# Performance work log

Measured on AMD Instinct MI355X. Metric: run time of the kernel, lower is better.

Reference implementation:

```python
import jax, jax.numpy as jnp
import numpy as np

EPS = 1e-8  # torch.cosine_similarity default eps


def _gru_stack(x_seq, h0, w_ih, w_hh, b_ih, b_hh):
    """Multi-layer GRU with input_size=hidden_size=1, vectorized over N lanes.
    x_seq: [T, N], h0: [L, N], w_ih/w_hh/b_ih/b_hh: [L, 3] (gate order r, z, n).
    Returns (last-layer output seq [T, N], final hidden per layer [L, N])."""
    def layer_body(x_seq, p):
        wi, wh, bi, bh, h0_l = p
        def step(h, x):
            r = jax.nn.sigmoid(wi[0] * x + bi[0] + wh[0] * h + bh[0])
            z = jax.nn.sigmoid(wi[1] * x + bi[1] + wh[1] * h + bh[1])
            n = jnp.tanh(wi[2] * x + bi[2] + r * (wh[2] * h + bh[2]))
            h_new = (1.0 - z) * n + z * h
            return h_new, h_new
        h_fin, out = jax.lax.scan(step, h0_l, x_seq)
        return out, h_fin
    out_seq, h_fin = jax.lax.scan(layer_body, x_seq, (w_ih, w_hh, b_ih, b_hh, h0))
    return out_seq, h_fin


def _forward(inputs, w_ih, w_hh, b_ih, b_hh, horizon):
    B, _, nodes, T = inputs.shape
    L = w_ih.shape[0]  # == T (num_layers = seq_len)
    # [B,1,nodes,T] -> [T, nodes, B] -> [T, nodes*B]; GRU weights are shared
    # across nodes, so all per-node GRU calls batch into one.
    x = inputs[:, 0].transpose(2, 1, 0).reshape(T, nodes * B)
    h0 = jnp.zeros((L, nodes * B), inputs.dtype)
    out, h = _gru_stack(x, h0, w_ih, w_hh, b_ih, b_hh)
    # horizon-1 additional passes, feeding output back as input with carried h
    def hstep(carry, _):
        o, hh = carry
        o, hh = _gru_stack(o, hh, w_ih, w_hh, b_ih, b_hh)
        return (o, hh), None
    (out, h), _ = jax.lax.scan(hstep, (out, h), None, length=horizon - 1)
    hv = h.reshape(L, nodes, B)  # final hidden scalar per (layer, node, batch)
    # cosine similarity across the batch dim between every pair of nodes
    norms = jnp.maximum(jnp.linalg.norm(hv, axis=-1), EPS)  # [L, nodes]
    dots = jnp.einsum('lib,ljb->lij', hv, hv)               # [L, nodes, nodes]
    adj = dots / (norms[:, :, None] * norms[:, None, :])
    # h0_gru list-of-per-node tensors [L, B, 1] -> stacked [nodes, L, B, 1]
    h_out = hv.transpose(1, 0, 2)[..., None]
    return adj, h_out


def setup_inputs() -> dict:
    key = jax.random.key(0)
    ks = jax.random.split(key, 5)
    B, nodes, T, horizon = 16, 1024, 24, 8
    inputs = jax.random.normal(ks[0], (B, 1, nodes, T), dtype=jnp.float32)
    # PyTorch GRU init: U(-1/sqrt(hidden), 1/sqrt(hidden)) = U(-1, 1) here
    u = lambda k: jax.random.uniform(k, (T, 3), dtype=jnp.float32, minval=-1.0, maxval=1.0)
    return {"inputs": inputs, "w_ih": u(ks[1]), "w_hh": u(ks[2]),
            "b_ih": u(ks[3]), "b_hh": u(ks[4]), "horizon": horizon}


def reference(inputs, w_ih, w_hh, b_ih, b_hh, horizon):
    return _forward(inputs, w_ih, w_hh, b_ih, b_hh, horizon)
```

## Files before the change

kernel.cpp:

```cpp
#include <hip/hip_runtime.h>
#include <math.h>

#define NODES 1024
#define BATCH 16
#define TLEN 24
#define LAYERS 24
#define NLANES (NODES * BATCH)
#define LOG2E 1.44269504088896340736f

typedef float v2f __attribute__((ext_vector_type(2)));

#if __has_builtin(__builtin_amdgcn_rcpf)
__device__ __forceinline__ float fast_rcp(float x) { return __builtin_amdgcn_rcpf(x); }
#else
__device__ __forceinline__ float fast_rcp(float x) { return 1.0f / x; }
#endif

#if __has_builtin(__builtin_amdgcn_exp2f)
__device__ __forceinline__ float fast_exp2(float x) { return __builtin_amdgcn_exp2f(x); }
#else
__device__ __forceinline__ float fast_exp2(float x) { return exp2f(x); }
#endif

#if __has_builtin(__builtin_elementwise_fma)
__device__ __forceinline__ v2f pk_fma(v2f a, v2f b, v2f c) {
    return __builtin_elementwise_fma(a, b, c);
}
#else
__device__ __forceinline__ v2f pk_fma(v2f a, v2f b, v2f c) {
    v2f d; d.x = fmaf(a.x, b.x, c.x); d.y = fmaf(a.y, b.y, c.y); return d;
}
#endif

struct GruK2 { v2f rW, rU, rC, zW, zU, zC, nW, nC, nU, nD; };
struct GruKs { float rW, rU, rC, zW, zU, zC, nW, nC, nU, nD; };

__device__ __forceinline__ GruK2 make_k2(
    const float* __restrict__ w_ih, const float* __restrict__ w_hh,
    const float* __restrict__ b_ih, const float* __restrict__ b_hh,
    int la, int lb)
{
    GruK2 K;
    #pragma unroll
    for (int s = 0; s < 2; ++s) {
        const int l = s ? lb : la;
        K.rW[s] = -LOG2E * w_ih[l*3+0]; K.rU[s] = -LOG2E * w_hh[l*3+0];
        K.rC[s] = -LOG2E * (b_ih[l*3+0] + b_hh[l*3+0]);
        K.zW[s] = -LOG2E * w_ih[l*3+1]; K.zU[s] = -LOG2E * w_hh[l*3+1];
        K.zC[s] = -LOG2E * (b_ih[l*3+1] + b_hh[l*3+1]);
        K.nW[s] = -2.0f*LOG2E * w_ih[l*3+2]; K.nC[s] = -2.0f*LOG2E * b_ih[l*3+2];
        K.nU[s] = -2.0f*LOG2E * w_hh[l*3+2]; K.nD[s] = -2.0f*LOG2E * b_hh[l*3+2];
    }
    return K;
}

__device__ __forceinline__ GruKs make_ks(
    const float* __restrict__ w_ih, const float* __restrict__ w_hh,
    const float* __restrict__ b_ih, const float* __restrict__ b_hh, int l)
{
    GruKs K;
    K.rW = -LOG2E * w_ih[l*3+0]; K.rU = -LOG2E * w_hh[l*3+0];
    K.rC = -LOG2E * (b_ih[l*3+0] + b_hh[l*3+0]);
    K.zW = -LOG2E * w_ih[l*3+1]; K.zU = -LOG2E * w_hh[l*3+1];
    K.zC = -LOG2E * (b_ih[l*3+1] + b_hh[l*3+1]);
    K.nW = -2.0f*LOG2E * w_ih[l*3+2]; K.nC = -2.0f*LOG2E * b_ih[l*3+2];
    K.nU = -2.0f*LOG2E * w_hh[l*3+2]; K.nD = -2.0f*LOG2E * b_hh[l*3+2];
    return K;
}

__device__ __forceinline__ v2f gru_cell2(const GruK2& K, v2f h, v2f xin) {
    const v2f ONE = (v2f){1.0f, 1.0f};
    v2f ar = pk_fma(K.rU, h, pk_fma(K.rW, xin, K.rC));
    v2f az = pk_fma(K.zU, h, pk_fma(K.zW, xin, K.zC));
    v2f er; er.x = fast_exp2(ar.x); er.y = fast_exp2(ar.y);
    v2f ez; ez.x = fast_exp2(az.x); ez.y = fast_exp2(az.y);
    v2f er1 = er + ONE;
    v2f r;  r.x = fast_rcp(er1.x); r.y = fast_rcp(er1.y);
    v2f an = pk_fma(r, pk_fma(K.nU, h, K.nD), pk_fma(K.nW, xin, K.nC));
    v2f en; en.x = fast_exp2(an.x); en.y = fast_exp2(an.y);
    v2f num = pk_fma(en, h - ez, h + ez);
    v2f den = (ez + ONE) * (en + ONE);
    v2f rd; rd.x = fast_rcp(den.x); rd.y = fast_rcp(den.y);
    return num * rd;
}

__device__ __forceinline__ float gru_cells(const GruKs& K, float h, float xin) {
    float ar = fmaf(K.rU, h, fmaf(K.rW, xin, K.rC));
    float az = fmaf(K.zU, h, fmaf(K.zW, xin, K.zC));
    float er = fast_exp2(ar);
    float ez = fast_exp2(az);
    float r  = fast_rcp(1.0f + er);
    float an = fmaf(r, fmaf(K.nU, h, K.nD), fmaf(K.nW, xin, K.nC));
    float en = fast_exp2(an);
    float num = fmaf(en, h - ez, h + ez);
    float den = (1.0f + ez) * (1.0f + en);
    return num * fast_rcp(den);
}

__global__ __launch_bounds__(256, 2) void gru_pipe_kernel(
    const float* __restrict__ inputs, const float* __restrict__ w_ih,
    const float* __restrict__ w_hh, const float* __restrict__ b_ih,
    const float* __restrict__ b_hh, const int* __restrict__ horizon_p,
    float* __restrict__ hv, float* __restrict__ h_out)
{
    __shared__ float xl[32][TLEN + 1];
    const int tid = threadIdx.x;
    const int wid = tid >> 6;
    const int lane = tid & 63;
    const int ring = lane >> 3;
    const int sl = lane & 7;
    const int L0 = 3 * sl;
    const int chain_local = wid * 8 + ring;
    const int c = blockIdx.x * 32 + chain_local;

    const GruK2 K01 = make_k2(w_ih, w_hh, b_ih, b_hh, L0, L0 + 1);
    const GruKs K2  = make_ks(w_ih, w_hh, b_ih, b_hh, L0 + 2);

    for (int i = tid; i < 32 * TLEN; i += 256) {
        const int cl = i / TLEN, t = i - cl * TLEN;
        const int cc = blockIdx.x * 32 + cl;
        const int node = cc >> 4, b = cc & 15;
        xl[cl][t] = inputs[((size_t)b * NODES + node) * TLEN + t];
    }
    __syncthreads();

    const int H = *horizon_p;
    const int last = H * TLEN;
    const int ringsrc = (lane & 56) | ((sl + 7) & 7);
    const bool lead = (sl == 0);
    const float* xrow = &xl[chain_local][0];

    v2f h01 = (v2f){0.0f, 0.0f};
    float h2 = 0.0f;
    float rel = 0.0f;

    for (int k = 0; k < TLEN; ++k) {
        v2f in01; in01.x = lead ? xrow[k] : rel; in01.y = h01.x;
        float p1 = h01.y;
        v2f n01 = gru_cell2(K01, h01, in01);
        float n2 = gru_cells(K2, h2, p1);
        h01.x = (k >= L0 + 0) ? n01.x : h01.x;
        h01.y = (k >= L0 + 1) ? n01.y : h01.y;
        h2    = (k >= L0 + 2) ? n2   : h2;
        rel = __shfl(h2, ringsrc, 64);
    }
    #pragma unroll 8
    for (int k = TLEN; k < last; ++k) {
        float p1 = h01.y;
        v2f in01; in01.x = rel; in01.y = h01.x;
        h2 = gru_cells(K2, h2, p1);
        rel = __shfl(h2, ringsrc, 64);
        h01 = gru_cell2(K01, h01, in01);
    }
    for (int k = last; k < last + LAYERS - 1; ++k) {
        v2f in01; in01.x = rel; in01.y = h01.x;
        float p1 = h01.y;
        v2f n01 = gru_cell2(K01, h01, in01);
        float n2 = gru_cells(K2, h2, p1);
        h01.x = (k < L0 + 0 + last) ? n01.x : h01.x;
        h01.y = (k < L0 + 1 + last) ? n01.y : h01.y;
        h2    = (k < L0 + 2 + last) ? n2   : h2;
        rel = __shfl(h2, ringsrc, 64);
    }

    const int node = c >> 4, b = c & 15;
    float* ho = h_out + (size_t)node * (LAYERS * BATCH) + b;
    hv[(size_t)(L0 + 0) * NLANES + c] = h01.x;  ho[(L0 + 0) * BATCH] = h01.x;
    hv[(size_t)(L0 + 1) * NLANES + c] = h01.y;  ho[(L0 + 1) * BATCH] = h01.y;
    hv[(size_t)(L0 + 2) * NLANES + c] = h2;     ho[(L0 + 2) * BATCH] = h2;
}

__global__ __launch_bounds__(256) void adj_kernel(
    const float* __restrict__ hv, float* __restrict__ adj)
{
    const int l = blockIdx.z;
    const int i0 = blockIdx.y * 64;
    const int j0 = blockIdx.x * 64;
    __shared__ float As[64 * 16];
    __shared__ float Bt[16 * 64];
    __shared__ float iA[64];
    __shared__ float iB[64];
    const int tid = threadIdx.x;
    const float* hvl = hv + (size_t)l * NLANES;

    ((float4*)As)[tid] = ((const float4*)(hvl + (size_t)i0 * 16))[tid];
    {
        const int j = tid >> 2;
        const int kc = (tid & 3) * 4;
        float4 bv = *(const float4*)(hvl + (size_t)(j0 + j) * 16 + kc);
        Bt[(kc + 0) * 64 + j] = bv.x;
        Bt[(kc + 1) * 64 + j] = bv.y;
        Bt[(kc + 2) * 64 + j] = bv.z;
        Bt[(kc + 3) * 64 + j] = bv.w;
    }
    __syncthreads();

    if (tid < 64) {
        float s = 0.0f;
        #pragma unroll
        for (int k = 0; k < 16; ++k) { float v = As[tid * 16 + k]; s = fmaf(v, v, s); }
        iA[tid] = fast_rcp(fmaxf(sqrtf(s), 1e-8f));
    } else if (tid < 128) {
        const int j = tid - 64;
        float s = 0.0f;
        #pragma unroll
        for (int k = 0; k < 16; ++k) { float v = Bt[k * 64 + j]; s = fmaf(v, v, s); }
        iB[j] = fast_rcp(fmaxf(sqrtf(s), 1e-8f));
    }
    __syncthreads();

    const int ty = tid >> 4;
    const int tx = tid & 15;

    float4 acc0 = {0,0,0,0}, acc1 = {0,0,0,0}, acc2 = {0,0,0,0}, acc3 = {0,0,0,0};
    #pragma unroll
    for (int kk = 0; kk < 4; ++kk) {
        float4 a0 = ((const float4*)As)[(ty * 4 + 0) * 4 + kk];
        float4 a1 = ((const float4*)As)[(ty * 4 + 1) * 4 + kk];
        float4 a2 = ((const float4*)As)[(ty * 4 + 2) * 4 + kk];
        float4 a3 = ((const float4*)As)[(ty * 4 + 3) * 4 + kk];
        #pragma unroll
        for (int e = 0; e < 4; ++e) {
            const int k = kk * 4 + e;
            float4 bk = ((const float4*)Bt)[k * 16 + tx];
            const float a0e = (e == 0) ? a0.x : (e == 1) ? a0.y : (e == 2) ? a0.z : a0.w;
            const float a1e = (e == 0) ? a1.x : (e == 1) ? a1.y : (e == 2) ? a1.z : a1.w;
            const float a2e = (e == 0) ? a2.x : (e == 1) ? a2.y : (e == 2) ? a2.z : a2.w;
            const float a3e = (e == 0) ? a3.x : (e == 1) ? a3.y : (e == 2) ? a3.z : a3.w;
            acc0.x = fmaf(a0e, bk.x, acc0.x); acc0.y = fmaf(a0e, bk.y, acc0.y);
            acc0.z = fmaf(a0e, bk.z, acc0.z); acc0.w = fmaf(a0e, bk.w, acc0.w);
            acc1.x = fmaf(a1e, bk.x, acc1.x); acc1.y = fmaf(a1e, bk.y, acc1.y);
            acc1.z = fmaf(a1e, bk.z, acc1.z); acc1.w = fmaf(a1e, bk.w, acc1.w);
            acc2.x = fmaf(a2e, bk.x, acc2.x); acc2.y = fmaf(a2e, bk.y, acc2.y);
            acc2.z = fmaf(a2e, bk.z, acc2.z); acc2.w = fmaf(a2e, bk.w, acc2.w);
            acc3.x = fmaf(a3e, bk.x, acc3.x); acc3.y = fmaf(a3e, bk.y, acc3.y);
            acc3.z = fmaf(a3e, bk.z, acc3.z); acc3.w = fmaf(a3e, bk.w, acc3.w);
        }
    }

    float* out = adj + (size_t)l * NODES * NODES;
    const float4 ib4 = ((const float4*)iB)[tx];
    #pragma unroll
    for (int ii = 0; ii < 4; ++ii) {
        const int i = i0 + ty * 4 + ii;
        const float si = iA[ty * 4 + ii];
        float4 a = (ii == 0) ? acc0 : (ii == 1) ? acc1 : (ii == 2) ? acc2 : acc3;
        float4 w;
        w.x = a.x * si * ib4.x;
        w.y = a.y * si * ib4.y;
        w.z = a.z * si * ib4.z;
        w.w = a.w * si * ib4.w;
        *(float4*)(out + (size_t)i * NODES + j0 + tx * 4) = w;
    }
}

extern "C" void kernel_launch(void* const* d_in, const int* in_sizes, int n_in,
                              void* d_out, int out_size, void* d_ws, size_t ws_size,
                              hipStream_t stream) {
    const float* inputs = (const float*)d_in[0];
    const float* w_ih   = (const float*)d_in[1];
    const float* w_hh   = (const float*)d_in[2];
    const float* b_ih   = (const float*)d_in[3];
    const float* b_hh   = (const float*)d_in[4];
    const int*   horiz  = (const int*)d_in[5];

    float* adj   = (float*)d_out;
    float* h_out = (float*)d_out + (size_t)LAYERS * NODES * NODES;
    float* hv    = (float*)d_ws;

    gru_pipe_kernel<<<NLANES / 32, 256, 0, stream>>>(inputs, w_ih, w_hh, b_ih, b_hh,
                                                     horiz, hv, h_out);

    dim3 grid(NODES / 64, NODES / 64, LAYERS);
    adj_kernel<<<grid, 256, 0, stream>>>(hv, adj);
}
```

Baseline: 76.36 us.

## Split GRU cell into two phases and vary loop schedule across alternating waves

Splits each GRU cell update into a gate-exponential phase and a finishing phase, interleaving the packed two-layer and scalar-layer work within each phase. The steady-state loop gets two code variants chosen by block and wave parity; one is rotated so the next step's first phase follows the finishing phase. The goal is to mix transcendental and FMA instructions better and to stagger waves sharing a SIMD. Unlike before, the lane shuffle now runs after all three layers update, so its latency may no longer hide behind the layer-0/1 work.

```diff
diff --git a/kernel.cpp b/kernel.cpp
--- a/kernel.cpp
+++ b/kernel.cpp
@@ -68,33 +68,43 @@
     return K;
 }
 
-__device__ __forceinline__ v2f gru_cell2(const GruK2& K, v2f h, v2f xin) {
+struct TickSt { v2f er01, ez01, in01; float er2, ez2, in2; };
+
+__device__ __forceinline__ TickSt part1(const GruK2& K01, const GruKs& K2,
+                                        v2f h01, float h2, float xa)
+{
+    TickSt S;
+    S.in01.x = xa; S.in01.y = h01.x;
+    S.in2 = h01.y;
+    float ar2 = fmaf(K2.rU, h2, fmaf(K2.rW, S.in2, K2.rC));
+    float az2 = fmaf(K2.zU, h2, fmaf(K2.zW, S.in2, K2.zC));
+    v2f ar01 = pk_fma(K01.rU, h01, pk_fma(K01.rW, S.in01, K01.rC));
+    v2f az01 = pk_fma(K01.zU, h01, pk_fma(K01.zW, S.in01, K01.zC));
+    S.er2 = fast_exp2(ar2);
+    S.ez2 = fast_exp2(az2);
+    S.er01.x = fast_exp2(ar01.x); S.er01.y = fast_exp2(ar01.y);
+    S.ez01.x = fast_exp2(az01.x); S.ez01.y = fast_exp2(az01.y);
+    return S;
+}
+
+__device__ __forceinline__ void part2(const GruK2& K01, const GruKs& K2,
+                                      const TickSt& S, v2f& h01, float& h2)
+{
     const v2f ONE = (v2f){1.0f, 1.0f};
-    v2f ar = pk_fma(K.rU, h, pk_fma(K.rW, xin, K.rC));
-    v2f az = pk_fma(K.zU, h, pk_fma(K.zW, xin, K.zC));
-    v2f er; er.x = fast_exp2(ar.x); er.y = fast_exp2(ar.y);
-    v2f ez; ez.x = fast_exp2(az.x); ez.y = fast_exp2(az.y);
-    v2f er1 = er + ONE;
-    v2f r;  r.x = fast_rcp(er1.x); r.y = fast_rcp(er1.y);
-    v2f an = pk_fma(r, pk_fma(K.nU, h, K.nD), pk_fma(K.nW, xin, K.nC));
-    v2f en; en.x = fast_exp2(an.x); en.y = fast_exp2(an.y);
-    v2f num = pk_fma(en, h - ez, h + ez);
-    v2f den = (ez + ONE) * (en + ONE);
-    v2f rd; rd.x = fast_rcp(den.x); rd.y = fast_rcp(den.y);
-    return num * rd;
-}
-
-__device__ __forceinline__ float gru_cells(const GruKs& K, float h, float xin) {
-    float ar = fmaf(K.rU, h, fmaf(K.rW, xin, K.rC));
-    float az = fmaf(K.zU, h, fmaf(K.zW, xin, K.zC));
-    float er = fast_exp2(ar);
-    float ez = fast_exp2(az);
-    float r  = fast_rcp(1.0f + er);
-    float an = fmaf(r, fmaf(K.nU, h, K.nD), fmaf(K.nW, xin, K.nC));
-    float en = fast_exp2(an);
-    float num = fmaf(en, h - ez, h + ez);
-    float den = (1.0f + ez) * (1.0f + en);
-    return num * fast_rcp(den);
+    float r2 = fast_rcp(1.0f + S.er2);
+    v2f e1 = S.er01 + ONE;
+    v2f r01; r01.x = fast_rcp(e1.x); r01.y = fast_rcp(e1.y);
+    float an2 = fmaf(r2, fmaf(K2.nU, h2, K2.nD), fmaf(K2.nW, S.in2, K2.nC));
+    v2f an01 = pk_fma(r01, pk_fma(K01.nU, h01, K01.nD), pk_fma(K01.nW, S.in01, K01.nC));
+    float en2 = fast_exp2(an2);
+    v2f en01; en01.x = fast_exp2(an01.x); en01.y = fast_exp2(an01.y);
+    float num2 = fmaf(en2, h2 - S.ez2, h2 + S.ez2);
+    float den2 = (1.0f + S.ez2) * (1.0f + en2);
+    h2 = num2 * fast_rcp(den2);
+    v2f num01 = pk_fma(en01, h01 - S.ez01, h01 + S.ez01);
+    v2f den01 = (S.ez01 + ONE) * (en01 + ONE);
+    v2f rd; rd.x = fast_rcp(den01.x); rd.y = fast_rcp(den01.y);
+    h01 = num01 * rd;
 }
 
 __global__ __launch_bounds__(256, 2) void gru_pipe_kernel(
@@ -135,31 +145,40 @@
     float rel = 0.0f;
 
     for (int k = 0; k < TLEN; ++k) {
-        v2f in01; in01.x = lead ? xrow[k] : rel; in01.y = h01.x;
-        float p1 = h01.y;
-        v2f n01 = gru_cell2(K01, h01, in01);
-        float n2 = gru_cells(K2, h2, p1);
-        h01.x = (k >= L0 + 0) ? n01.x : h01.x;
-        h01.y = (k >= L0 + 1) ? n01.y : h01.y;
-        h2    = (k >= L0 + 2) ? n2   : h2;
+        float inA = lead ? xrow[k] : rel;
+        TickSt S = part1(K01, K2, h01, h2, inA);
+        v2f th01 = h01; float th2 = h2;
+        part2(K01, K2, S, th01, th2);
+        h01.x = (k >= L0 + 0) ? th01.x : h01.x;
+        h01.y = (k >= L0 + 1) ? th01.y : h01.y;
+        h2    = (k >= L0 + 2) ? th2   : h2;
         rel = __shfl(h2, ringsrc, 64);
     }
-    #pragma unroll 8
-    for (int k = TLEN; k < last; ++k) {
-        float p1 = h01.y;
-        v2f in01; in01.x = rel; in01.y = h01.x;
-        h2 = gru_cells(K2, h2, p1);
+    if (((blockIdx.x + wid) & 1) == 0) {
+        #pragma unroll 4
+        for (int k = TLEN; k < last; ++k) {
+            TickSt S = part1(K01, K2, h01, h2, rel);
+            part2(K01, K2, S, h01, h2);
+            rel = __shfl(h2, ringsrc, 64);
+        }
+    } else {
+        TickSt S = part1(K01, K2, h01, h2, rel);
+        #pragma unroll 4
+        for (int k = TLEN; k < last - 1; ++k) {
+            part2(K01, K2, S, h01, h2);
+            rel = __shfl(h2, ringsrc, 64);
+            S = part1(K01, K2, h01, h2, rel);
+        }
+        part2(K01, K2, S, h01, h2);
         rel = __shfl(h2, ringsrc, 64);
-        h01 = gru_cell2(K01, h01, in01);
     }
     for (int k = last; k < last + LAYERS - 1; ++k) {
-        v2f in01; in01.x = rel; in01.y = h01.x;
-        float p1 = h01.y;
-        v2f n01 = gru_cell2(K01, h01, in01);
-        float n2 = gru_cells(K2, h2, p1);
-        h01.x = (k < L0 + 0 + last) ? n01.x : h01.x;
-        h01.y = (k < L0 + 1 + last) ? n01.y : h01.y;
-        h2    = (k < L0 + 2 + last) ? n2   : h2;
+        TickSt S = part1(K01, K2, h01, h2, rel);
+        v2f th01 = h01; float th2 = h2;
+        part2(K01, K2, S, th01, th2);
+        h01.x = (k < L0 + 0 + last) ? th01.x : h01.x;
+        h01.y = (k < L0 + 1 + last) ? th01.y : h01.y;
+        h2    = (k < L0 + 2 + last) ? th2   : h2;
         rel = __shfl(h2, ringsrc, 64);
     }
 
```

New measurement: 77.47 us. About the same (+1.5%).
